# Kernel optimization log

Hardware: AMD Instinct MI355X
Metric: run time of the kernel (lower is better)

Reference implementation:

```python
import jax, jax.numpy as jnp
import numpy as np

B, T, NE = 2, 2048, 1024
NH, NKV, HD = 16, 4, 64
GC = 32  # ve_gate_channels
WIN = 1024  # sliding window (left)
EPS = 1e-6


def rope(x, cos, sin):
    # x: (B,T,H,D), cos/sin: (B,T,D//2)
    cos = cos[:, :, None, :]
    sin = sin[:, :, None, :]
    x1, x2 = jnp.split(x, 2, axis=-1)
    return jnp.concatenate([x1 * cos + x2 * sin, -x1 * sin + x2 * cos], axis=-1)


def rmsnorm(x):
    return x * jax.lax.rsqrt(jnp.mean(x * x, axis=-1, keepdims=True) + EPS)


def setup_inputs() -> dict:
    key = jax.random.key(0)
    ks = jax.random.split(key, 7)
    x = jax.random.normal(ks[0], (B, T, NE), jnp.float32)
    ve = jax.random.normal(ks[1], (B, T, NKV * HD), jnp.float32)
    # real RoPE tables (already 'sliced to correct positions')
    inv_freq = 1.0 / (10000.0 ** (jnp.arange(HD // 2, dtype=jnp.float32) / (HD // 2)))
    ang = jnp.arange(T, dtype=jnp.float32)[:, None] * inv_freq[None, :]  # (T, D//2)
    cos = jnp.broadcast_to(jnp.cos(ang)[None], (B, T, HD // 2))
    sin = jnp.broadcast_to(jnp.sin(ang)[None], (B, T, HD // 2))
    s = 0.02
    Wq = jax.random.normal(ks[2], (NE, NH * HD), jnp.float32) * s
    Wk = jax.random.normal(ks[3], (NE, NKV * HD), jnp.float32) * s
    Wv = jax.random.normal(ks[4], (NE, NKV * HD), jnp.float32) * s
    Wo = jax.random.normal(ks[5], (NE, NE), jnp.float32) * s
    Wg = jax.random.normal(ks[6], (GC, NKV), jnp.float32) * s
    return {"x": x, "ve": ve, "cos": cos, "sin": sin,
            "Wq": Wq, "Wk": Wk, "Wv": Wv, "Wo": Wo, "Wg": Wg,
            "window_size": WIN}


def reference(x, ve, cos, sin, Wq, Wk, Wv, Wo, Wg, window_size):
    Bs, Ts, _ = x.shape
    q = (x @ Wq).reshape(Bs, Ts, NH, HD)
    k = (x @ Wk).reshape(Bs, Ts, NKV, HD)
    v = (x @ Wv).reshape(Bs, Ts, NKV, HD)
    # gated value embeddings
    gate = 2.0 * jax.nn.sigmoid(x[..., :GC] @ Wg)  # (B,T,NKV)
    v = v + gate[..., None] * ve.reshape(Bs, Ts, NKV, HD)
    q = rmsnorm(rope(q, cos, sin))
    k = rmsnorm(rope(k, cos, sin))
    # GQA: head h uses kv head h // rep
    rep = NH // NKV
    k = jnp.repeat(k, rep, axis=2)
    v = jnp.repeat(v, rep, axis=2)
    scale = 1.0 / jnp.sqrt(jnp.float32(HD))
    scores = jnp.einsum('bthd,bshd->bhts', q, k) * scale  # (B,H,T,T)
    i = jnp.arange(Ts)[:, None]
    j = jnp.arange(Ts)[None, :]
    mask = (j <= i) & (i - j <= window_size)  # causal + sliding window
    scores = jnp.where(mask, scores, -jnp.inf)
    p = jax.nn.softmax(scores, axis=-1)
    y = jnp.einsum('bhts,bshd->bthd', p, v).reshape(Bs, Ts, NE)
    return y @ Wo
```

## Files before the change

### kernel.cpp

```cpp
#include <hip/hip_runtime.h>
#include <hip/hip_bf16.h>
#include <string.h>

typedef __attribute__((ext_vector_type(8))) short bf16x8;
typedef __attribute__((ext_vector_type(4))) short bf16x4;
typedef __attribute__((ext_vector_type(4))) float f32x4;
typedef __attribute__((ext_vector_type(4))) int i32x4;
typedef __attribute__((ext_vector_type(2))) int i32x2;

#define DEV __device__ __forceinline__
#define WIN_ 1024

DEV short f2bf(float f) {
  __hip_bfloat16 h = __float2bfloat16(f);
  short s; __builtin_memcpy(&s, &h, 2); return s;
}
DEV float bf2f(short s) {
  union { unsigned u; float f; } a; a.u = ((unsigned)(unsigned short)s) << 16;
  return a.f;
}
DEV unsigned pkbf2(float a, float b) {
  __hip_bfloat162 h = __float22bfloat162_rn(make_float2(a, b));
  unsigned u; __builtin_memcpy(&u, &h, 4); return u;
}
DEV float fexp2(float x) {
#if __has_builtin(__builtin_amdgcn_exp2f)
  return __builtin_amdgcn_exp2f(x);
#else
  return exp2f(x);
#endif
}

DEV f32x4 mfma16(bf16x4 a, bf16x4 b, f32x4 c) {
#if __has_builtin(__builtin_amdgcn_mfma_f32_16x16x16bf16_1k)
  return __builtin_amdgcn_mfma_f32_16x16x16bf16_1k(a, b, c, 0, 0, 0);
#else
  asm volatile("s_nop 1\n\tv_mfma_f32_16x16x16_bf16 %0, %1, %2, %0\n\ts_nop 7\n\ts_nop 7"
               : "+v"(c) : "v"(a), "v"(b));
  return c;
#endif
}

DEV void gload16(const short* g, short* l) {
  __builtin_amdgcn_global_load_lds((const __attribute__((address_space(1))) unsigned int*)g,
                                   (__attribute__((address_space(3))) unsigned int*)l,
                                   16, 0, 0);
}

__global__ __launch_bounds__(256) void k_prep(const float* __restrict__ x,
    const float* __restrict__ Wq, const float* __restrict__ Wk, const float* __restrict__ Wv,
    const float* __restrict__ Wo, short* __restrict__ xb, short* __restrict__ WbT,
    short* __restrict__ WoT) {
  const int bid = blockIdx.x;
  if (bid < 2048) {
    size_t i = ((size_t)bid * 256 + threadIdx.x) * 8;
    f32x4 v0 = *(const f32x4*)(x + i);
    f32x4 v1 = *(const f32x4*)(x + i + 4);
    i32x4 o = {(int)pkbf2(v0[0], v0[1]), (int)pkbf2(v0[2], v0[3]),
               (int)pkbf2(v1[0], v1[1]), (int)pkbf2(v1[2], v1[3])};
    *(i32x4*)(xb + i) = o;
    return;
  }
  int t = bid - 2048;
  const float* src; short* dst; int srcld, bx, by;
  if (t < 1024)      { src = Wq; dst = WbT;                        srcld = 1024; bx = t & 31;          by = t >> 5; }
  else if (t < 1280) { src = Wk; dst = WbT + (size_t)1024 * 1024;  srcld = 256;  bx = (t - 1024) & 7;  by = (t - 1024) >> 3; }
  else if (t < 1536) { src = Wv; dst = WbT + (size_t)1280 * 1024;  srcld = 256;  bx = (t - 1280) & 7;  by = (t - 1280) >> 3; }
  else               { src = Wo; dst = WoT;                        srcld = 1024; bx = (t - 1536) & 31; by = (t - 1536) >> 5; }
  __shared__ float tile[32][33];
  const int n0 = bx * 32, k0 = by * 32;
  const int tx = threadIdx.x & 31, ty = threadIdx.x >> 5;
#pragma unroll
  for (int i = 0; i < 4; ++i)
    tile[ty * 4 + i][tx] = src[(size_t)(k0 + ty * 4 + i) * srcld + n0 + tx];
  __syncthreads();
#pragma unroll
  for (int i = 0; i < 4; ++i)
    dst[(size_t)(n0 + ty * 4 + i) * 1024 + k0 + tx] = f2bf(tile[tx][ty * 4 + i]);
}

__global__ __launch_bounds__(256) void k_gemm_qkv(const short* __restrict__ A, const short* __restrict__ BT,
    const float* __restrict__ x, const float* __restrict__ ve,
    const float* __restrict__ cosp, const float* __restrict__ sinp, const float* __restrict__ Wg,
    short* __restrict__ qh, short* __restrict__ kh, short* __restrict__ vhT) {
  const int K = 1024;
  __shared__ short As[2][8192];
  __shared__ short Bs[2][4096];
  const int tid = threadIdx.x;
  const int l = tid & 63, w = tid >> 6;
  const int l15 = l & 15, hi = l >> 4;
  const int bid = blockIdx.x;
  const int wg = (bid & 7) * 96 + (bid >> 3);
  const int bx = wg % 24;
  const int m0 = (wg / 24) * 128, n0 = bx * 64;
  const int srow = tid >> 3;
  const int segsw = 8 * ((tid & 7) ^ (srow & 7));
  const int lo = tid * 8;
  const short* pa = A + (size_t)(m0 + srow) * K + segsw;
  const short* pb = BT + (size_t)(n0 + srow) * K + segsw;
  const int f8 = l15 & 7;

  f32x4 acc[2][4];
#pragma unroll
  for (int i = 0; i < 2; ++i)
#pragma unroll
    for (int j = 0; j < 4; ++j) acc[i][j] = (f32x4){0.f, 0.f, 0.f, 0.f};

  auto stage = [&](int buf, int koff) {
    gload16(pa + koff,          &As[buf][lo]);
    gload16(pa + 32 * K + koff, &As[buf][lo + 2048]);
    gload16(pa + 64 * K + koff, &As[buf][lo + 4096]);
    gload16(pa + 96 * K + koff, &As[buf][lo + 6144]);
    gload16(pb + koff,          &Bs[buf][lo]);
    gload16(pb + 32 * K + koff, &Bs[buf][lo + 2048]);
  };

  stage(0, 0);
  __syncthreads();
  int cur = 0;
  for (int k0 = 0; k0 < K; k0 += 64) {
    if (k0 + 64 < K) stage(cur ^ 1, k0 + 64);
    bf16x8 af[2][2], bfr[4][2];
#pragma unroll
    for (int c = 0; c < 2; ++c) {
      int seg = 8 * ((4 * c + hi) ^ f8);
#pragma unroll
      for (int mi = 0; mi < 2; ++mi)
        af[mi][c] = *(const bf16x8*)&As[cur][(32 * w + 16 * mi + l15) * 64 + seg];
#pragma unroll
      for (int ni = 0; ni < 4; ++ni)
        bfr[ni][c] = *(const bf16x8*)&Bs[cur][(16 * ni + l15) * 64 + seg];
    }
#pragma unroll
    for (int c = 0; c < 2; ++c)
#pragma unroll
      for (int mi = 0; mi < 2; ++mi)
#pragma unroll
        for (int ni = 0; ni < 4; ++ni)
          acc[mi][ni] = __builtin_amdgcn_mfma_f32_16x16x32_bf16(af[mi][c], bfr[ni][c], acc[mi][ni], 0, 0, 0);
    __syncthreads();
    cur ^= 1;
  }

  if (bx < 20) {
    short* dst0 = (bx < 16) ? qh : kh;
#pragma unroll
    for (int mi = 0; mi < 2; ++mi)
#pragma unroll
      for (int r = 0; r < 4; ++r) {
        int bt = m0 + 32 * w + 16 * mi + 4 * hi + r;
        int b = bt >> 11, t = bt & 2047;
        float c0 = cosp[bt * 32 + l15],      s0 = sinp[bt * 32 + l15];
        float c1 = cosp[bt * 32 + 16 + l15], s1 = sinp[bt * 32 + 16 + l15];
        float a0 = acc[mi][0][r], b0 = acc[mi][2][r];
        float a1 = acc[mi][1][r], b1 = acc[mi][3][r];
        float o0 = a0 * c0 + b0 * s0;
        float o2 = b0 * c0 - a0 * s0;
        float o1 = a1 * c1 + b1 * s1;
        float o3 = b1 * c1 - a1 * s1;
        float ss = o0 * o0 + o1 * o1 + o2 * o2 + o3 * o3;
        ss += __shfl_xor(ss, 1); ss += __shfl_xor(ss, 2);
        ss += __shfl_xor(ss, 4); ss += __shfl_xor(ss, 8);
        float rinv = rsqrtf(ss * (1.f / 64.f) + 1e-6f);
        if (bx < 16) rinv *= 0.18033688011112042f;
        size_t rb = ((size_t)((b * ((bx < 16) ? 16 : 4) + ((bx < 16) ? bx : bx - 16)) * 2048 + t)) * 64;
        dst0[rb + l15]      = f2bf(o0 * rinv);
        dst0[rb + 16 + l15] = f2bf(o1 * rinv);
        dst0[rb + 32 + l15] = f2bf(o2 * rinv);
        dst0[rb + 48 + l15] = f2bf(o3 * rinv);
      }
  } else {
    const int kvh = bx - 20;
#pragma unroll
    for (int mi = 0; mi < 2; ++mi)
#pragma unroll
      for (int r = 0; r < 4; ++r) {
        int bt = m0 + 32 * w + 16 * mi + 4 * hi + r;
        int b = bt >> 11, t = bt & 2047;
        const float* xr = x + (size_t)bt * 1024;
        float z = 0.f;
#pragma unroll
        for (int gg = 0; gg < 32; ++gg) z += xr[gg] * Wg[gg * 4 + kvh];
        float gate = 2.f / (1.f + __expf(-z));
        const float* vep = ve + (size_t)bt * 256 + kvh * 64;
        short* dst = vhT + (size_t)(b * 4 + kvh) * 131072 + t;
#pragma unroll
        for (int ni = 0; ni < 4; ++ni) {
          int d = 16 * ni + l15;
          float vv = acc[mi][ni][r] + gate * vep[d];
          dst[(size_t)d * 2048] = f2bf(vv);
        }
      }
  }
}

template <int LDC, bool F32OUT>
__global__ __launch_bounds__(256) void k_gemm_bt(const short* __restrict__ A, const short* __restrict__ BT,
                                                 void* __restrict__ Cv, int K) {
  __shared__ short As[2][8192];
  __shared__ short Bs[2][4096];
  const int tid = threadIdx.x;
  const int l = tid & 63, w = tid >> 6;
  const int l15 = l & 15, hi = l >> 4;
  const int bid = blockIdx.x;
  const int wg = (bid & 7) * 64 + (bid >> 3);
  const int m0 = (wg >> 4) * 128, n0 = (wg & 15) * 64;
  const int srow = tid >> 3;
  const int segsw = 8 * ((tid & 7) ^ (srow & 7));
  const int lo = tid * 8;
  const short* pa = A + (size_t)(m0 + srow) * K + segsw;
  const short* pb = BT + (size_t)(n0 + srow) * K + segsw;
  const int f8 = l15 & 7;

  f32x4 acc[2][4];
#pragma unroll
  for (int i = 0; i < 2; ++i)
#pragma unroll
    for (int j = 0; j < 4; ++j) acc[i][j] = (f32x4){0.f, 0.f, 0.f, 0.f};

  auto stage = [&](int buf, int koff) {
    gload16(pa + koff,          &As[buf][lo]);
    gload16(pa + 32 * K + koff, &As[buf][lo + 2048]);
    gload16(pa + 64 * K + koff, &As[buf][lo + 4096]);
    gload16(pa + 96 * K + koff, &As[buf][lo + 6144]);
    gload16(pb + koff,          &Bs[buf][lo]);
    gload16(pb + 32 * K + koff, &Bs[buf][lo + 2048]);
  };

  stage(0, 0);
  __syncthreads();
  int cur = 0;
  for (int k0 = 0; k0 < K; k0 += 64) {
    if (k0 + 64 < K) stage(cur ^ 1, k0 + 64);
    bf16x8 af[2][2], bfr[4][2];
#pragma unroll
    for (int c = 0; c < 2; ++c) {
      int seg = 8 * ((4 * c + hi) ^ f8);
#pragma unroll
      for (int mi = 0; mi < 2; ++mi)
        af[mi][c] = *(const bf16x8*)&As[cur][(32 * w + 16 * mi + l15) * 64 + seg];
#pragma unroll
      for (int ni = 0; ni < 4; ++ni)
        bfr[ni][c] = *(const bf16x8*)&Bs[cur][(16 * ni + l15) * 64 + seg];
    }
#pragma unroll
    for (int c = 0; c < 2; ++c)
#pragma unroll
      for (int mi = 0; mi < 2; ++mi)
#pragma unroll
        for (int ni = 0; ni < 4; ++ni)
          acc[mi][ni] = __builtin_amdgcn_mfma_f32_16x16x32_bf16(af[mi][c], bfr[ni][c], acc[mi][ni], 0, 0, 0);
    __syncthreads();
    cur ^= 1;
  }
#pragma unroll
  for (int mi = 0; mi < 2; ++mi)
#pragma unroll
    for (int ni = 0; ni < 4; ++ni)
#pragma unroll
      for (int r = 0; r < 4; ++r) {
        int crow = m0 + 32 * w + 16 * mi + 4 * hi + r;
        int ccol = n0 + 16 * ni + l15;
        if (F32OUT) ((float*)Cv)[(size_t)crow * LDC + ccol] = acc[mi][ni][r];
        else        ((short*)Cv)[(size_t)crow * LDC + ccol] = f2bf(acc[mi][ni][r]);
      }
}

__global__ __launch_bounds__(256) void k_attn(const short* __restrict__ qh, const short* __restrict__ kh,
                                              const short* __restrict__ vhT, short* __restrict__ yb) {
  __shared__ i32x4 lds4[2][1024];
  char* base = (char*)lds4;
  const int bid = blockIdx.x;
  const int kq = bid >> 8, low = bid & 255;
  const int h = low & 15, b = (low >> 4) & 1, q0 = low >> 5;
  const int qt = (kq == 0) ? (31 - q0) : (kq == 1) ? (16 + q0) : (kq == 2) ? (15 - q0) : q0;
  const int kvh = h >> 2;
  const int qs = qt * 64;
  const int tid = threadIdx.x;
  const int w = tid >> 6, l = tid & 63, l15 = l & 15, hi = l >> 4;
  const int qi = qs + 16 * w + l15;
  const int rsw = (l15 & 7) << 4;

  const short* qb = qh + ((size_t)((b * 16 + h) * 2048 + qs + 16 * w + l15)) * 64;
  bf16x8 qf0 = *(const bf16x8*)(qb + 8 * hi);
  bf16x8 qf1 = *(const bf16x8*)(qb + 32 + 8 * hi);

  f32x4 oacc[4];
#pragma unroll
  for (int i = 0; i < 4; ++i) oacc[i] = (f32x4){0.f, 0.f, 0.f, 0.f};
  f32x4 lsacc = (f32x4){0.f, 0.f, 0.f, 0.f};
  const bf16x4 vone = {(short)0x3F80, (short)0x3F80, (short)0x3F80, (short)0x3F80};

  const int kt_lo = (qs >= 1024) ? ((qs - 1024) >> 6) : 0;
  const int kt_hi = qs >> 6;
  const short* kbase = kh + ((size_t)(b * 4 + kvh) * 2048) * 64;
  const short* vbase = vhT + ((size_t)(b * 4 + kvh) * 64) * 2048;

  const int srow = tid >> 3, sseg = tid & 7;
  const int swz = (srow & 7) << 4;
  const int ko = ((srow << 7) + (sseg << 4)) ^ swz;
  const short* kp = kbase + (size_t)(kt_lo * 64 + srow) * 64 + sseg * 8;
  const short* vp = vbase + (size_t)srow * 2048 + kt_lo * 64 + sseg * 8;
  i32x4 rk0, rk1, rv0, rv1;

#define LOADT() do { \
    rk0 = *(const i32x4*)kp; \
    rk1 = *(const i32x4*)(kp + 2048); \
    rv0 = *(const i32x4*)vp; \
    rv1 = *(const i32x4*)(vp + 32 * 2048); \
  } while (0)

#define WRITET(DST) do { \
    char* kd = (DST); \
    *(i32x4*)(kd + ko) = rk0; \
    *(i32x4*)(kd + ko + 4096) = rk1; \
    char* vd = kd + 8192; \
    *(i32x4*)(vd + ko) = rv0; \
    *(i32x4*)(vd + ko + 4096) = rv1; \
  } while (0)

  auto TILE = [&](char* kbuf, int kt) {
    char* vbuf = kbuf + 8192;
    f32x4 s[4];
#pragma unroll
    for (int nt = 0; nt < 4; ++nt) s[nt] = (f32x4){0.f, 0.f, 0.f, 0.f};
#pragma unroll
    for (int c = 0; c < 2; ++c) {
      bf16x8 qc = c ? qf1 : qf0;
#pragma unroll
      for (int nt = 0; nt < 4; ++nt) {
        bf16x8 kf = *(const bf16x8*)(kbuf + ((((16 * nt + l15) << 7) + (c << 6) + (hi << 4)) ^ rsw));
        s[nt] = __builtin_amdgcn_mfma_f32_16x16x32_bf16(kf, qc, s[nt], 0, 0, 0);
      }
    }
    if (kt == kt_lo || kt == kt_hi) {
      const int k0 = kt * 64;
#pragma unroll
      for (int nt = 0; nt < 4; ++nt)
#pragma unroll
        for (int r = 0; r < 4; ++r) {
          int kj = k0 + 16 * nt + 4 * hi + r;
          if (kj > qi || (qi - kj) > WIN_) s[nt][r] = -1e30f;
        }
    }
#pragma unroll
    for (int nt = 0; nt < 4; ++nt)
#pragma unroll
      for (int r = 0; r < 4; ++r) s[nt][r] = fexp2(s[nt][r]);

    bf16x4 pa[4];
#pragma unroll
    for (int nt = 0; nt < 4; ++nt) {
      i32x2 pk = {(int)pkbf2(s[nt][0], s[nt][1]), (int)pkbf2(s[nt][2], s[nt][3])};
      pa[nt] = __builtin_bit_cast(bf16x4, pk);
    }
#pragma unroll
    for (int nt = 0; nt < 4; ++nt) lsacc = mfma16(vone, pa[nt], lsacc);
#pragma unroll
    for (int dt = 0; dt < 4; ++dt) {
      int rowb = ((16 * dt + l15) << 7) + (hi << 3);
#pragma unroll
      for (int nt = 0; nt < 4; ++nt) {
        i32x2 vv = *(const i32x2*)(vbuf + ((rowb + 32 * nt) ^ rsw));
        oacc[dt] = mfma16(__builtin_bit_cast(bf16x4, vv), pa[nt], oacc[dt]);
      }
    }
  };

  LOADT();
  WRITET(base);
  __syncthreads();

  int kt = kt_lo;
  for (;;) {
    if (kt < kt_hi) { kp += 4096; vp += 64; LOADT(); }
    __builtin_amdgcn_s_setprio(1);
    TILE(base, kt);
    __builtin_amdgcn_s_setprio(0);
    if (kt < kt_hi) WRITET(base + 16384);
    __syncthreads();
    if (kt == kt_hi) break;
    ++kt;
    if (kt < kt_hi) { kp += 4096; vp += 64; LOADT(); }
    __builtin_amdgcn_s_setprio(1);
    TILE(base + 16384, kt);
    __builtin_amdgcn_s_setprio(0);
    if (kt < kt_hi) WRITET(base);
    __syncthreads();
    if (kt == kt_hi) break;
    ++kt;
  }
#undef LOADT
#undef WRITET

  float inv = 1.f / lsacc[0];
  size_t orow = (size_t)(b * 2048 + qs + 16 * w + l15);
#pragma unroll
  for (int dt = 0; dt < 4; ++dt) {
    int col0 = h * 64 + 16 * dt + 4 * hi;
    i32x2 pk = {(int)pkbf2(oacc[dt][0] * inv, oacc[dt][1] * inv),
                (int)pkbf2(oacc[dt][2] * inv, oacc[dt][3] * inv)};
    *(i32x2*)(yb + orow * 1024 + col0) = pk;
  }
}

extern "C" void kernel_launch(void* const* d_in, const int* in_sizes, int n_in,
                              void* d_out, int out_size, void* d_ws, size_t ws_size,
                              hipStream_t stream) {
  const float* x    = (const float*)d_in[0];
  const float* ve   = (const float*)d_in[1];
  const float* cosp = (const float*)d_in[2];
  const float* sinp = (const float*)d_in[3];
  const float* Wq   = (const float*)d_in[4];
  const float* Wk   = (const float*)d_in[5];
  const float* Wv   = (const float*)d_in[6];
  const float* Wo   = (const float*)d_in[7];
  const float* Wg   = (const float*)d_in[8];
  float* out = (float*)d_out;

  char* ws = (char*)d_ws;
  short* xb   = (short*)(ws);
  short* WbT  = (short*)(ws + 8388608);
  short* WoT  = (short*)(ws + 11534336);
  short* qh   = (short*)(ws + 26214400);
  short* kh   = (short*)(ws + 34603008);
  short* vhT  = (short*)(ws + 36700160);
  short* yb   = (short*)(ws + 38797312);

  k_prep<<<4608, 256, 0, stream>>>(x, Wq, Wk, Wv, Wo, xb, WbT, WoT);

  k_gemm_qkv<<<768, 256, 0, stream>>>(xb, WbT, x, ve, cosp, sinp, Wg, qh, kh, vhT);

  k_attn<<<1024, 256, 0, stream>>>(qh, kh, vhT, yb);

  k_gemm_bt<1024, true><<<512, 256, 0, stream>>>(yb, WoT, out, 1024);
}
```

Before: 83.27 us.

## Software-pipeline QK^T of next tile with softmax/PV of previous tile

Splits the attention tile body into a QK^T stage and a mask/exp/PV stage. The loop now computes scores for tile k while finishing tile k-1, so MFMA work and the exp/VALU work can interleave. This adds a second __syncthreads per iteration, a loop-carried copy of the score registers and more register pressure. It also delays the LDS write of the next tile until after the previous buffer is consumed.

```diff
diff --git a/kernel.cpp b/kernel.cpp
--- a/kernel.cpp
+++ b/kernel.cpp
@@ -319,9 +319,7 @@
     *(i32x4*)(vd + ko + 4096) = rv1; \
   } while (0)
 
-  auto TILE = [&](char* kbuf, int kt) {
-    char* vbuf = kbuf + 8192;
-    f32x4 s[4];
+  auto QKF = [&](char* kbuf, f32x4 (&s)[4]) {
 #pragma unroll
     for (int nt = 0; nt < 4; ++nt) s[nt] = (f32x4){0.f, 0.f, 0.f, 0.f};
 #pragma unroll
@@ -333,8 +331,12 @@
         s[nt] = __builtin_amdgcn_mfma_f32_16x16x32_bf16(kf, qc, s[nt], 0, 0, 0);
       }
     }
-    if (kt == kt_lo || kt == kt_hi) {
-      const int k0 = kt * 64;
+  };
+
+  auto FINISH = [&](f32x4 (&s)[4], int ktX, char* kbuf) {
+    char* vbuf = kbuf + 8192;
+    if (ktX == kt_lo || ktX == kt_hi) {
+      const int k0 = ktX * 64;
 #pragma unroll
       for (int nt = 0; nt < 4; ++nt)
 #pragma unroll
@@ -347,7 +349,6 @@
     for (int nt = 0; nt < 4; ++nt)
 #pragma unroll
       for (int r = 0; r < 4; ++r) s[nt][r] = fexp2(s[nt][r]);
-
     bf16x4 pa[4];
 #pragma unroll
     for (int nt = 0; nt < 4; ++nt) {
@@ -371,25 +372,35 @@
   WRITET(base);
   __syncthreads();
 
+  f32x4 sP[4], sC[4];
+  QKF(base, sP);
+  int ktP = kt_lo;
   int kt = kt_lo;
-  for (;;) {
+  if (kt < kt_hi) {
+    kp += 4096; vp += 64; LOADT();
+    WRITET(base + 16384);
+  }
+  __syncthreads();
+
+  while (kt < kt_hi) {
+    ++kt;
+    const int par = (kt - kt_lo) & 1;
+    char* bufC = base + par * 16384;
+    char* bufP = base + (par ^ 1) * 16384;
     if (kt < kt_hi) { kp += 4096; vp += 64; LOADT(); }
     __builtin_amdgcn_s_setprio(1);
-    TILE(base, kt);
+    QKF(bufC, sC);
     __builtin_amdgcn_s_setprio(0);
-    if (kt < kt_hi) WRITET(base + 16384);
+    FINISH(sP, ktP, bufP);
     __syncthreads();
-    if (kt == kt_hi) break;
-    ++kt;
-    if (kt < kt_hi) { kp += 4096; vp += 64; LOADT(); }
-    __builtin_amdgcn_s_setprio(1);
-    TILE(base + 16384, kt);
-    __builtin_amdgcn_s_setprio(0);
-    if (kt < kt_hi) WRITET(base);
+    if (kt < kt_hi) WRITET(bufP);
     __syncthreads();
-    if (kt == kt_hi) break;
-    ++kt;
-  }
+#pragma unroll
+    for (int nt = 0; nt < 4; ++nt) sP[nt] = sC[nt];
+    ktP = kt;
+  }
+  FINISH(sP, ktP, base + (((ktP - kt_lo) & 1)) * 16384);
+
 #undef LOADT
 #undef WRITET
 
```

Result: slower. 85.43 us (+2.6%).
